# Kernel optimization log

Measured on AMD Instinct MI355X. Metric: run time of the kernel, lower is better.

Reference implementation:

```python
import jax, jax.numpy as jnp
import numpy as np
import math

B, S, E, NH = 1024, 16, 32, 4  # batch, seq, attn embed dim, heads
H = 64                          # lstm1 hidden; lstm2 hidden = H//2 = E


def _pos_encoding(s, d):
    pos = jnp.arange(s, dtype=jnp.float32)[:, None]
    div = jnp.exp(jnp.arange(0, d, 2, dtype=jnp.float32) * (-math.log(10000.0) / d))
    pe = jnp.zeros((s, d), jnp.float32)
    pe = pe.at[:, 0::2].set(jnp.sin(pos * div))
    pe = pe.at[:, 1::2].set(jnp.cos(pos * div))
    return pe


def _lstm(x, wih, whh, bih, bhh):
    # x: [B,S,in]; PyTorch gate order i,f,g,o; h0=c0=0
    b = x.shape[0]
    h_dim = whh.shape[1]
    xg = jnp.einsum('bsi,gi->bsg', x, wih) + bih + bhh  # precompute input contribution

    def step(carry, xt):
        h, c = carry
        g = xt + h @ whh.T
        i, f, gg, o = jnp.split(g, 4, axis=-1)
        c = jax.nn.sigmoid(f) * c + jax.nn.sigmoid(i) * jnp.tanh(gg)
        h = jax.nn.sigmoid(o) * jnp.tanh(c)
        return (h, c), h

    h0 = jnp.zeros((b, h_dim), x.dtype)
    _, hs = jax.lax.scan(step, (h0, h0), jnp.swapaxes(xg, 0, 1))
    return jnp.swapaxes(hs, 0, 1)  # [B,S,H]


def setup_inputs() -> dict:
    key = jax.random.key(0)
    ks = jax.random.split(key, 24)

    def rn(k, shape, s=0.15):
        return jax.random.normal(k, shape, jnp.float32) * s

    return {
        'x': jax.random.normal(ks[0], (B, S, 1), jnp.float32),
        'emb_w': rn(ks[1], (32, 1)), 'emb_b': rn(ks[2], (32,), 0.05),
        'l1_wih': rn(ks[3], (4 * H, 32)), 'l1_whh': rn(ks[4], (4 * H, H)),
        'l1_bih': rn(ks[5], (4 * H,), 0.05), 'l1_bhh': rn(ks[6], (4 * H,), 0.05),
        'l2_wih': rn(ks[7], (4 * (H // 2), H)), 'l2_whh': rn(ks[8], (4 * (H // 2), H // 2)),
        'l2_bih': rn(ks[9], (4 * (H // 2),), 0.05), 'l2_bhh': rn(ks[10], (4 * (H // 2),), 0.05),
        'attn_w': rn(ks[11], (3 * E, E)), 'attn_b': rn(ks[12], (3 * E,), 0.05),
        'attn_ow': rn(ks[13], (E, E)), 'attn_ob': rn(ks[14], (E,), 0.05),
        'd1_w': rn(ks[15], (64, E)), 'd1_b': rn(ks[16], (64,), 0.05),
        'bn1_g': jnp.ones((64,), jnp.float32), 'bn1_b': jnp.zeros((64,), jnp.float32),
        'd2_w': rn(ks[17], (32, 64)), 'd2_b': rn(ks[18], (32,), 0.05),
        'bn2_g': jnp.ones((32,), jnp.float32), 'bn2_b': jnp.zeros((32,), jnp.float32),
        'd3_w': rn(ks[19], (1, 32)), 'd3_b': rn(ks[20], (1,), 0.05),
    }


def reference(x, emb_w, emb_b, l1_wih, l1_whh, l1_bih, l1_bhh,
              l2_wih, l2_whh, l2_bih, l2_bhh,
              attn_w, attn_b, attn_ow, attn_ob,
              d1_w, d1_b, bn1_g, bn1_b, d2_w, d2_b, bn2_g, bn2_b, d3_w, d3_b):
    eps = 1e-5
    h = x @ emb_w.T + emb_b                      # [B,S,32]
    h = h + _pos_encoding(h.shape[1], h.shape[2])
    l1 = _lstm(h, l1_wih, l1_whh, l1_bih, l1_bhh)          # [B,S,64]  (dropout: eval -> id)
    l2 = _lstm(l1, l2_wih, l2_whh, l2_bih, l2_bhh)         # [B,S,32]
    l2 = l2 + l1[:, :, :l2.shape[2]]                        # residual

    # nn.MultiheadAttention with default batch_first=False: attends over axis 0 (=B here),
    # faithful to the original module's behavior.
    L, N, _ = l2.shape
    hd = E // NH
    qkv = l2 @ attn_w.T + attn_b
    q, k, v = jnp.split(qkv, 3, axis=-1)
    q = q.reshape(L, N, NH, hd) * (1.0 / math.sqrt(hd))
    k = k.reshape(L, N, NH, hd)
    v = v.reshape(L, N, NH, hd)
    scores = jnp.einsum('lnhd,mnhd->nhlm', q, k)           # [S,4,B,B]
    a = jax.nn.softmax(scores, axis=-1)
    att = jnp.einsum('nhlm,mnhd->lnhd', a, v).reshape(L, N, E)
    att = att @ attn_ow.T + attn_ob

    z = att[:, -1, :]                                       # [B,32]

    def bn(t, g, b):  # eval-mode BatchNorm1d with fresh running stats (mean=0, var=1)
        return t * (g / jnp.sqrt(1.0 + eps)) + b

    z = jax.nn.relu(bn(z @ d1_w.T + d1_b, bn1_g, bn1_b))
    z = jax.nn.relu(bn(z @ d2_w.T + d2_b, bn2_g, bn2_b))
    return jax.nn.sigmoid(z @ d3_w.T + d3_b)                # [B,1]
```

## Files before the change

### kernel.cpp

```cpp
#include <hip/hip_runtime.h>
#include <math.h>


typedef __attribute__((ext_vector_type(8))) short short8v;
typedef __attribute__((ext_vector_type(4))) float f32x4;

__device__ __forceinline__ float sigf(float x) { return 1.0f / (1.0f + __expf(-x)); }
__device__ __forceinline__ float tanh_f(float x) {
    float a = fabsf(x);
    float e = __expf(2.0f * a);
    float t = 1.0f - 2.0f / (e + 1.0f);
    return copysignf(t, x);
}
__device__ __forceinline__ unsigned short f2bf(float f) {
    unsigned int u = __float_as_uint(f);
    unsigned int r = (u + 0x7FFFu + ((u >> 16) & 1u)) >> 16;
    return (unsigned short)r;
}

__global__ __launch_bounds__(256, 1) void lstm_kernel(
    const float* __restrict__ x,
    const float* __restrict__ emb_w, const float* __restrict__ emb_b,
    const float* __restrict__ wih1, const float* __restrict__ whh1,
    const float* __restrict__ bih1, const float* __restrict__ bhh1,
    const float* __restrict__ wih2, const float* __restrict__ whh2,
    const float* __restrict__ bih2, const float* __restrict__ bhh2,
    const float* __restrict__ attn_w, const float* __restrict__ attn_b,
    float* __restrict__ Q, float* __restrict__ K, float* __restrict__ V) {
    const int tid = threadIdx.x;
    const int w = tid >> 6, lane = tid & 63;
    const int l15 = lane & 15, q4 = lane >> 4;
    const int base = blockIdx.x * 16;

    __shared__ __align__(16) unsigned char E_raw[16 * 1024];
    __shared__ __align__(16) unsigned char H1_raw[2][2048];
    __shared__ __align__(16) unsigned char H2_raw[2][1024];
    __shared__ __align__(16) unsigned char WF2[24 * 1024];
    __shared__ __align__(16) float L1F[16][64];
    __shared__ __align__(16) float L2F[16][32];

    const unsigned jx7 = (unsigned)(l15 & 7) << 4;
    const unsigned jx4 = (unsigned)(l15 & 3) << 4;

    short8v w1f[4][3];
#pragma unroll
    for (int t = 0; t < 4; t++) {
        const int row = (w + 4 * t) * 16 + l15;
#pragma unroll
        for (int sl = 0; sl < 3; sl++) {
            short8v f;
#pragma unroll
            for (int e = 0; e < 8; e++) {
                int k = sl * 32 + q4 * 8 + e;
                float v = (k < 64) ? whh1[row * 64 + k] : wih1[row * 32 + (k - 64)];
                f[e] = (short)f2bf(v);
            }
            w1f[t][sl] = f;
        }
    }

    for (int f = w; f < 24; f += 4) {
        int t2 = f / 3, sl = f - t2 * 3;
        int row = t2 * 16 + l15;
        int koff = sl * 32 + q4 * 8;
        const float* src = (sl < 2) ? (wih2 + row * 64 + koff) : (whh2 + row * 32 + (koff - 64));
        float4 va = *(const float4*)(src);
        float4 vb = *(const float4*)(src + 4);
        short8v pk;
        pk[0] = (short)f2bf(va.x); pk[1] = (short)f2bf(va.y);
        pk[2] = (short)f2bf(va.z); pk[3] = (short)f2bf(va.w);
        pk[4] = (short)f2bf(vb.x); pk[5] = (short)f2bf(vb.y);
        pk[6] = (short)f2bf(vb.z); pk[7] = (short)f2bf(vb.w);
        *(short8v*)(&WF2[f * 1024 + lane * 16]) = pk;
    }

    float b1r[4][4];
#pragma unroll
    for (int t = 0; t < 4; t++)
#pragma unroll
        for (int e = 0; e < 4; e++) {
            int r = (w + 4 * t) * 16 + q4 * 4 + e;
            b1r[t][e] = bih1[r] + bhh1[r];
        }
    float b2r[4][4];
#pragma unroll
    for (int t = 0; t < 4; t++)
#pragma unroll
        for (int e = 0; e < 4; e++) {
            int r = ((w & 1) + 2 * t) * 16 + q4 * 4 + e;
            b2r[t][e] = bih2[r] + bhh2[r];
        }

    *(unsigned long long*)(H1_raw[0] + tid * 8) = 0ULL;
    if (tid < 128) *(unsigned long long*)(H2_raw[0] + tid * 8) = 0ULL;
    {
        const int je = tid >> 4, se = tid & 15;
        float xv = x[(base + je) * 16 + se];
        float ev[32];
#pragma unroll
        for (int ii = 0; ii < 16; ii++) {
            float d = __expf(-0.28782313662425574f * (float)(2 * ii));
            float ang = (float)se * d;
            ev[2 * ii] = xv * emb_w[2 * ii] + emb_b[2 * ii] + __sinf(ang);
            ev[2 * ii + 1] = xv * emb_w[2 * ii + 1] + emb_b[2 * ii + 1] + __cosf(ang);
        }
        unsigned jm = (unsigned)(je & 3) << 4;
#pragma unroll
        for (int b = 0; b < 4; b++) {
            short8v pk;
#pragma unroll
            for (int e = 0; e < 8; e++) pk[e] = (short)f2bf(ev[b * 8 + e]);
            *(short8v*)(&E_raw[se * 1024 + je * 64 + (((unsigned)(b * 16)) ^ jm)]) = pk;
        }
    }
    float c1[4] = {0.f, 0.f, 0.f, 0.f};
    float c2[4] = {0.f, 0.f, 0.f, 0.f};
    __syncthreads();

    const int u0 = w * 16 + q4 * 4;
    const int u20 = w * 16 + q4 * 4;

#define L2FRAG(T, SL) (*(const short8v*)(&WF2[(((w + 2 * (T)) * 3 + (SL)) << 10) + lane * 16]))

#pragma unroll 2
    for (int s = 0; s < 16; s++) {
        const int p = s & 1, pn = p ^ 1;
        const unsigned char* H1p = H1_raw[p];
        unsigned char* H1n = H1_raw[pn];
        short8v B0 = *(const short8v*)(H1p + (((unsigned)(l15 * 128 + q4 * 16)) ^ jx7));
        short8v B1 = *(const short8v*)(H1p + (((unsigned)(l15 * 128 + 64 + q4 * 16)) ^ jx7));
        short8v BE = *(const short8v*)(&E_raw[s * 1024] + (((unsigned)(l15 * 64 + q4 * 16)) ^ jx4));
        f32x4 a0 = {b1r[0][0], b1r[0][1], b1r[0][2], b1r[0][3]};
        f32x4 a1 = {b1r[1][0], b1r[1][1], b1r[1][2], b1r[1][3]};
        f32x4 a2 = {b1r[2][0], b1r[2][1], b1r[2][2], b1r[2][3]};
        f32x4 a3 = {b1r[3][0], b1r[3][1], b1r[3][2], b1r[3][3]};
        a0 = __builtin_amdgcn_mfma_f32_16x16x32_bf16(w1f[0][0], B0, a0, 0, 0, 0);
        a1 = __builtin_amdgcn_mfma_f32_16x16x32_bf16(w1f[1][0], B0, a1, 0, 0, 0);
        a2 = __builtin_amdgcn_mfma_f32_16x16x32_bf16(w1f[2][0], B0, a2, 0, 0, 0);
        a3 = __builtin_amdgcn_mfma_f32_16x16x32_bf16(w1f[3][0], B0, a3, 0, 0, 0);
        a0 = __builtin_amdgcn_mfma_f32_16x16x32_bf16(w1f[0][1], B1, a0, 0, 0, 0);
        a1 = __builtin_amdgcn_mfma_f32_16x16x32_bf16(w1f[1][1], B1, a1, 0, 0, 0);
        a2 = __builtin_amdgcn_mfma_f32_16x16x32_bf16(w1f[2][1], B1, a2, 0, 0, 0);
        a3 = __builtin_amdgcn_mfma_f32_16x16x32_bf16(w1f[3][1], B1, a3, 0, 0, 0);
        a0 = __builtin_amdgcn_mfma_f32_16x16x32_bf16(w1f[0][2], BE, a0, 0, 0, 0);
        a1 = __builtin_amdgcn_mfma_f32_16x16x32_bf16(w1f[1][2], BE, a1, 0, 0, 0);
        a2 = __builtin_amdgcn_mfma_f32_16x16x32_bf16(w1f[2][2], BE, a2, 0, 0, 0);
        a3 = __builtin_amdgcn_mfma_f32_16x16x32_bf16(w1f[3][2], BE, a3, 0, 0, 0);
        float h1v[4];
#pragma unroll
        for (int e = 0; e < 4; e++) {
            c1[e] = sigf(a1[e]) * c1[e] + sigf(a0[e]) * tanh_f(a2[e]);
            h1v[e] = sigf(a3[e]) * tanh_f(c1[e]);
        }
        {
            unsigned long long pk =
                (unsigned long long)f2bf(h1v[0]) | ((unsigned long long)f2bf(h1v[1]) << 16) |
                ((unsigned long long)f2bf(h1v[2]) << 32) | ((unsigned long long)f2bf(h1v[3]) << 48);
            *(unsigned long long*)(H1n + (((unsigned)(l15 * 128 + u0 * 2)) ^ jx7)) = pk;
        }
        if (s == 15) *(float4*)(&L1F[l15][u0]) = make_float4(h1v[0], h1v[1], h1v[2], h1v[3]);
        __syncthreads();
        if (w < 2) {
            const unsigned char* H2p = H2_raw[p];
            short8v C0 = *(const short8v*)(H1n + (((unsigned)(l15 * 128 + q4 * 16)) ^ jx7));
            short8v C1f = *(const short8v*)(H1n + (((unsigned)(l15 * 128 + 64 + q4 * 16)) ^ jx7));
            short8v C2 = *(const short8v*)(H2p + (((unsigned)(l15 * 64 + q4 * 16)) ^ jx4));
            f32x4 d0 = {b2r[0][0], b2r[0][1], b2r[0][2], b2r[0][3]};
            f32x4 d1 = {b2r[1][0], b2r[1][1], b2r[1][2], b2r[1][3]};
            f32x4 d2 = {b2r[2][0], b2r[2][1], b2r[2][2], b2r[2][3]};
            f32x4 d3 = {b2r[3][0], b2r[3][1], b2r[3][2], b2r[3][3]};
            d0 = __builtin_amdgcn_mfma_f32_16x16x32_bf16(L2FRAG(0, 0), C0, d0, 0, 0, 0);
            d1 = __builtin_amdgcn_mfma_f32_16x16x32_bf16(L2FRAG(1, 0), C0, d1, 0, 0, 0);
            d2 = __builtin_amdgcn_mfma_f32_16x16x32_bf16(L2FRAG(2, 0), C0, d2, 0, 0, 0);
            d3 = __builtin_amdgcn_mfma_f32_16x16x32_bf16(L2FRAG(3, 0), C0, d3, 0, 0, 0);
            d0 = __builtin_amdgcn_mfma_f32_16x16x32_bf16(L2FRAG(0, 1), C1f, d0, 0, 0, 0);
            d1 = __builtin_amdgcn_mfma_f32_16x16x32_bf16(L2FRAG(1, 1), C1f, d1, 0, 0, 0);
            d2 = __builtin_amdgcn_mfma_f32_16x16x32_bf16(L2FRAG(2, 1), C1f, d2, 0, 0, 0);
            d3 = __builtin_amdgcn_mfma_f32_16x16x32_bf16(L2FRAG(3, 1), C1f, d3, 0, 0, 0);
            d0 = __builtin_amdgcn_mfma_f32_16x16x32_bf16(L2FRAG(0, 2), C2, d0, 0, 0, 0);
            d1 = __builtin_amdgcn_mfma_f32_16x16x32_bf16(L2FRAG(1, 2), C2, d1, 0, 0, 0);
            d2 = __builtin_amdgcn_mfma_f32_16x16x32_bf16(L2FRAG(2, 2), C2, d2, 0, 0, 0);
            d3 = __builtin_amdgcn_mfma_f32_16x16x32_bf16(L2FRAG(3, 2), C2, d3, 0, 0, 0);
            float h2v[4];
#pragma unroll
            for (int e = 0; e < 4; e++) {
                c2[e] = sigf(d1[e]) * c2[e] + sigf(d0[e]) * tanh_f(d2[e]);
                h2v[e] = sigf(d3[e]) * tanh_f(c2[e]);
            }
            unsigned long long pk =
                (unsigned long long)f2bf(h2v[0]) | ((unsigned long long)f2bf(h2v[1]) << 16) |
                ((unsigned long long)f2bf(h2v[2]) << 32) | ((unsigned long long)f2bf(h2v[3]) << 48);
            *(unsigned long long*)(H2_raw[pn] + (((unsigned)(l15 * 64 + u20 * 2)) ^ jx4)) = pk;
            if (s == 15) *(float4*)(&L2F[l15][u20]) = make_float4(h2v[0], h2v[1], h2v[2], h2v[3]);
        }
        __syncthreads();
    }

    {
        const int j = tid >> 4, rb = tid & 15;
        const int gb = base + j;
        const float4* l1p = (const float4*)(&L1F[j][0]);
        const float4* l2p = (const float4*)(&L2F[j][0]);
#pragma unroll
        for (int rep = 0; rep < 6; rep++) {
            int row = rb + 16 * rep;
            float acc = attn_b[row];
            const float4* wrow = (const float4*)(attn_w + row * 32);
#pragma unroll
            for (int k4 = 0; k4 < 8; k4++) {
                float4 lv1 = l1p[k4];
                float4 lv2 = l2p[k4];
                float4 ww = wrow[k4];
                float lx = lv2.x + lv1.x, ly = lv2.y + lv1.y, lz = lv2.z + lv1.z, lw = lv2.w + lv1.w;
                acc += lx * ww.x + ly * ww.y + lz * ww.z + lw * ww.w;
            }
            if (row < 32) Q[gb * 32 + row] = acc * 0.35355339059327373f;
            else if (row < 64) K[gb * 32 + (row - 32)] = acc;
            else V[gb * 32 + (row - 64)] = acc;
        }
    }
#undef L2FRAG
}

__global__ __launch_bounds__(256, 2) void attn_kernel(
    const float* __restrict__ Q, const float* __restrict__ K, const float* __restrict__ V,
    float* __restrict__ pm, float* __restrict__ ps, float* __restrict__ pacc) {
    int c = blockIdx.x & 15, lt = blockIdx.x >> 4;
    int t = threadIdx.x;
    int h = t >> 6, l = lt * 64 + (t & 63);
    __shared__ __align__(16) float Ks[64 * 32];
    __shared__ __align__(16) float Vs[64 * 32];
    {
        const float4* Kg = (const float4*)(K + c * 2048);
        const float4* Vg = (const float4*)(V + c * 2048);
        float4* K4 = (float4*)Ks;
        float4* V4 = (float4*)Vs;
        K4[t] = Kg[t];
        K4[t + 256] = Kg[t + 256];
        V4[t] = Vg[t];
        V4[t + 256] = Vg[t + 256];
    }
    const float4* qg = (const float4*)(Q + l * 32 + h * 8);
    float4 q0 = qg[0], q1 = qg[1];
    __syncthreads();
    float m_r = -1e30f, l_r = 0.f;
    float4 acc0 = {0, 0, 0, 0}, acc1 = {0, 0, 0, 0};
#pragma unroll 4
    for (int m = 0; m < 64; m++) {
        const float4* k4 = (const float4*)(Ks + m * 32 + h * 8);
        float4 ka = k4[0], kb = k4[1];
        float s = q0.x * ka.x + q0.y * ka.y + q0.z * ka.z + q0.w * ka.w +
                  q1.x * kb.x + q1.y * kb.y + q1.z * kb.z + q1.w * kb.w;
        const float4* v4 = (const float4*)(Vs + m * 32 + h * 8);
        float4 va = v4[0], vb = v4[1];
        float nm = fmaxf(m_r, s);
        float f = __expf(m_r - nm);
        float pp = __expf(s - nm);
        l_r = l_r * f + pp;
        acc0.x = acc0.x * f + pp * va.x;
        acc0.y = acc0.y * f + pp * va.y;
        acc0.z = acc0.z * f + pp * va.z;
        acc0.w = acc0.w * f + pp * va.w;
        acc1.x = acc1.x * f + pp * vb.x;
        acc1.y = acc1.y * f + pp * vb.y;
        acc1.z = acc1.z * f + pp * vb.z;
        acc1.w = acc1.w * f + pp * vb.w;
        m_r = nm;
    }
    int idx = (c * 4 + h) * 1024 + l;
    pm[idx] = m_r;
    ps[idx] = l_r;
    float4* po = (float4*)(pacc + idx * 8);
    po[0] = acc0;
    po[1] = acc1;
}

__global__ __launch_bounds__(256) void head_kernel(
    const float* __restrict__ pm, const float* __restrict__ ps, const float* __restrict__ pacc,
    const float* __restrict__ ow, const float* __restrict__ ob,
    const float* __restrict__ d1w, const float* __restrict__ d1b,
    const float* __restrict__ g1, const float* __restrict__ b1,
    const float* __restrict__ d2w, const float* __restrict__ d2b,
    const float* __restrict__ g2, const float* __restrict__ b2,
    const float* __restrict__ d3w, const float* __restrict__ d3b,
    float* __restrict__ out) {
    int wid = threadIdx.x >> 6, j = threadIdx.x & 63;
    int l = blockIdx.x * 4 + wid;
    __shared__ float att_s[4][32], z_s[4][32], r1s[4][64];
    if (j < 32) {
        int h = j >> 3, d = j & 7;
        float M = -1e30f;
#pragma unroll
        for (int c = 0; c < 16; c++) M = fmaxf(M, pm[(c * 4 + h) * 1024 + l]);
        float den = 0.f, num = 0.f;
#pragma unroll
        for (int c = 0; c < 16; c++) {
            int idx = (c * 4 + h) * 1024 + l;
            float e = __expf(pm[idx] - M);
            den += e * ps[idx];
            num += e * pacc[idx * 8 + d];
        }
        att_s[wid][j] = num / den;
    }
    __syncthreads();
    if (j < 32) {
        float a = ob[j];
#pragma unroll
        for (int i = 0; i < 32; i++) a += att_s[wid][i] * ow[j * 32 + i];
        z_s[wid][j] = a;
    }
    __syncthreads();
    const float inv = rsqrtf(1.0f + 1e-5f);
    if (j < 64) {
        float a = d1b[j];
#pragma unroll
        for (int i = 0; i < 32; i++) a += z_s[wid][i] * d1w[j * 32 + i];
        a = a * (g1[j] * inv) + b1[j];
        r1s[wid][j] = fmaxf(a, 0.f);
    }
    __syncthreads();
    if (j < 32) {
        float a = d2b[j];
#pragma unroll
        for (int i = 0; i < 64; i++) a += r1s[wid][i] * d2w[j * 64 + i];
        a = a * (g2[j] * inv) + b2[j];
        float r2 = fmaxf(a, 0.f);
        float p = r2 * d3w[j];
        p += __shfl_down(p, 16);
        p += __shfl_down(p, 8);
        p += __shfl_down(p, 4);
        p += __shfl_down(p, 2);
        p += __shfl_down(p, 1);
        if (j == 0) out[l] = 1.0f / (1.0f + __expf(-(p + d3b[0])));
    }
}

extern "C" void kernel_launch(void* const* d_in, const int* in_sizes, int n_in,
                              void* d_out, int out_size, void* d_ws, size_t ws_size,
                              hipStream_t stream) {
    const float* x      = (const float*)d_in[0];
    const float* emb_w  = (const float*)d_in[1];
    const float* emb_b  = (const float*)d_in[2];
    const float* l1_wih = (const float*)d_in[3];
    const float* l1_whh = (const float*)d_in[4];
    const float* l1_bih = (const float*)d_in[5];
    const float* l1_bhh = (const float*)d_in[6];
    const float* l2_wih = (const float*)d_in[7];
    const float* l2_whh = (const float*)d_in[8];
    const float* l2_bih = (const float*)d_in[9];
    const float* l2_bhh = (const float*)d_in[10];
    const float* attn_w = (const float*)d_in[11];
    const float* attn_b = (const float*)d_in[12];
    const float* attn_ow = (const float*)d_in[13];
    const float* attn_ob = (const float*)d_in[14];
    const float* d1_w  = (const float*)d_in[15];
    const float* d1_b  = (const float*)d_in[16];
    const float* bn1_g = (const float*)d_in[17];
    const float* bn1_b = (const float*)d_in[18];
    const float* d2_w  = (const float*)d_in[19];
    const float* d2_b  = (const float*)d_in[20];
    const float* bn2_g = (const float*)d_in[21];
    const float* bn2_b = (const float*)d_in[22];
    const float* d3_w  = (const float*)d_in[23];
    const float* d3_b  = (const float*)d_in[24];
    float* out = (float*)d_out;

    float* ws   = (float*)d_ws;
    float* Q    = ws;
    float* K    = ws + 32768;
    float* V    = ws + 65536;
    float* pm   = ws + 98304;
    float* ps   = ws + 163840;
    float* pacc = ws + 229376;

    lstm_kernel<<<64, 256, 0, stream>>>(x, emb_w, emb_b, l1_wih, l1_whh, l1_bih, l1_bhh,
                                        l2_wih, l2_whh, l2_bih, l2_bhh,
                                        attn_w, attn_b, Q, K, V);
    attn_kernel<<<256, 256, 0, stream>>>(Q, K, V, pm, ps, pacc);
    head_kernel<<<256, 256, 0, stream>>>(pm, ps, pacc, attn_ow, attn_ob, d1_w, d1_b,
                                         bn1_g, bn1_b, d2_w, d2_b, bn2_g, bn2_b,
                                         d3_w, d3_b, out);
}
```

Before: 162.5 us.

## Skew LSTM layers to one barrier per step and fuse attention with head

The LSTM loop is restructured so that layer 2 at step s runs alongside layer 1 at step s+1. Both read the same H1 buffer, which removes one of the two barriers per timestep and lets layer 2 reuse layer 1's loaded fragments. The attention and head kernels are merged into one kernel in which each wave scans all keys directly from global memory and reduces the partial softmax states with shuffles, removing the partial-result buffers and one launch. Sigmoid and tanh now use the hardware reciprocal, and bf16 packing uses v_cvt_pk_bf16_f32; both change rounding slightly, and the fused attention now reads K and V from global/L2 in every block.

```diff
diff --git a/kernel.cpp b/kernel.cpp
--- a/kernel.cpp
+++ b/kernel.cpp
@@ -5,17 +5,25 @@
 typedef __attribute__((ext_vector_type(8))) short short8v;
 typedef __attribute__((ext_vector_type(4))) float f32x4;
 
-__device__ __forceinline__ float sigf(float x) { return 1.0f / (1.0f + __expf(-x)); }
+__device__ __forceinline__ float sigf(float x) {
+    float e = __expf(-x);
+    return __builtin_amdgcn_rcpf(1.0f + e);
+}
 __device__ __forceinline__ float tanh_f(float x) {
     float a = fabsf(x);
     float e = __expf(2.0f * a);
-    float t = 1.0f - 2.0f / (e + 1.0f);
+    float t = 1.0f - 2.0f * __builtin_amdgcn_rcpf(e + 1.0f);
     return copysignf(t, x);
 }
 __device__ __forceinline__ unsigned short f2bf(float f) {
     unsigned int u = __float_as_uint(f);
     unsigned int r = (u + 0x7FFFu + ((u >> 16) & 1u)) >> 16;
     return (unsigned short)r;
+}
+__device__ __forceinline__ unsigned cvtpk_bf16(float lo, float hi) {
+    unsigned r;
+    asm("v_cvt_pk_bf16_f32 %0, %1, %2" : "=v"(r) : "v"(lo), "v"(hi));
+    return r;
 }
 
 __global__ __launch_bounds__(256, 1) void lstm_kernel(
@@ -91,8 +99,8 @@
             b2r[t][e] = bih2[r] + bhh2[r];
         }
 
-    *(unsigned long long*)(H1_raw[0] + tid * 8) = 0ULL;
-    if (tid < 128) *(unsigned long long*)(H2_raw[0] + tid * 8) = 0ULL;
+    *(unsigned long long*)(H1_raw[1] + tid * 8) = 0ULL;
+    if (tid < 128) *(unsigned long long*)(H2_raw[1] + tid * 8) = 0ULL;
     {
         const int je = tid >> 4, se = tid & 15;
         float xv = x[(base + je) * 16 + se];
@@ -115,25 +123,24 @@
     }
     float c1[4] = {0.f, 0.f, 0.f, 0.f};
     float c2[4] = {0.f, 0.f, 0.f, 0.f};
-    __syncthreads();
 
     const int u0 = w * 16 + q4 * 4;
-    const int u20 = w * 16 + q4 * 4;
-
+
+#define LDBE(S)  (*(const short8v*)(&E_raw[(S) * 1024] + (((unsigned)(l15 * 64 + q4 * 16)) ^ jx4)))
+#define LDB0(HP) (*(const short8v*)((HP) + (((unsigned)(l15 * 128 + q4 * 16)) ^ jx7)))
+#define LDB1(HP) (*(const short8v*)((HP) + (((unsigned)(l15 * 128 + 64 + q4 * 16)) ^ jx7)))
+#define LDC2(HP) (*(const short8v*)((HP) + (((unsigned)(l15 * 64 + q4 * 16)) ^ jx4)))
 #define L2FRAG(T, SL) (*(const short8v*)(&WF2[(((w + 2 * (T)) * 3 + (SL)) << 10) + lane * 16]))
 
-#pragma unroll 2
-    for (int s = 0; s < 16; s++) {
-        const int p = s & 1, pn = p ^ 1;
-        const unsigned char* H1p = H1_raw[p];
-        unsigned char* H1n = H1_raw[pn];
-        short8v B0 = *(const short8v*)(H1p + (((unsigned)(l15 * 128 + q4 * 16)) ^ jx7));
-        short8v B1 = *(const short8v*)(H1p + (((unsigned)(l15 * 128 + 64 + q4 * 16)) ^ jx7));
-        short8v BE = *(const short8v*)(&E_raw[s * 1024] + (((unsigned)(l15 * 64 + q4 * 16)) ^ jx4));
+    auto phase1 = [&](unsigned char* H1n, short8v BE, short8v B0, short8v B1, bool last) {
         f32x4 a0 = {b1r[0][0], b1r[0][1], b1r[0][2], b1r[0][3]};
         f32x4 a1 = {b1r[1][0], b1r[1][1], b1r[1][2], b1r[1][3]};
         f32x4 a2 = {b1r[2][0], b1r[2][1], b1r[2][2], b1r[2][3]};
         f32x4 a3 = {b1r[3][0], b1r[3][1], b1r[3][2], b1r[3][3]};
+        a0 = __builtin_amdgcn_mfma_f32_16x16x32_bf16(w1f[0][2], BE, a0, 0, 0, 0);
+        a1 = __builtin_amdgcn_mfma_f32_16x16x32_bf16(w1f[1][2], BE, a1, 0, 0, 0);
+        a2 = __builtin_amdgcn_mfma_f32_16x16x32_bf16(w1f[2][2], BE, a2, 0, 0, 0);
+        a3 = __builtin_amdgcn_mfma_f32_16x16x32_bf16(w1f[3][2], BE, a3, 0, 0, 0);
         a0 = __builtin_amdgcn_mfma_f32_16x16x32_bf16(w1f[0][0], B0, a0, 0, 0, 0);
         a1 = __builtin_amdgcn_mfma_f32_16x16x32_bf16(w1f[1][0], B0, a1, 0, 0, 0);
         a2 = __builtin_amdgcn_mfma_f32_16x16x32_bf16(w1f[2][0], B0, a2, 0, 0, 0);
@@ -142,41 +149,41 @@
         a1 = __builtin_amdgcn_mfma_f32_16x16x32_bf16(w1f[1][1], B1, a1, 0, 0, 0);
         a2 = __builtin_amdgcn_mfma_f32_16x16x32_bf16(w1f[2][1], B1, a2, 0, 0, 0);
         a3 = __builtin_amdgcn_mfma_f32_16x16x32_bf16(w1f[3][1], B1, a3, 0, 0, 0);
-        a0 = __builtin_amdgcn_mfma_f32_16x16x32_bf16(w1f[0][2], BE, a0, 0, 0, 0);
-        a1 = __builtin_amdgcn_mfma_f32_16x16x32_bf16(w1f[1][2], BE, a1, 0, 0, 0);
-        a2 = __builtin_amdgcn_mfma_f32_16x16x32_bf16(w1f[2][2], BE, a2, 0, 0, 0);
-        a3 = __builtin_amdgcn_mfma_f32_16x16x32_bf16(w1f[3][2], BE, a3, 0, 0, 0);
         float h1v[4];
 #pragma unroll
         for (int e = 0; e < 4; e++) {
             c1[e] = sigf(a1[e]) * c1[e] + sigf(a0[e]) * tanh_f(a2[e]);
             h1v[e] = sigf(a3[e]) * tanh_f(c1[e]);
         }
-        {
-            unsigned long long pk =
-                (unsigned long long)f2bf(h1v[0]) | ((unsigned long long)f2bf(h1v[1]) << 16) |
-                ((unsigned long long)f2bf(h1v[2]) << 32) | ((unsigned long long)f2bf(h1v[3]) << 48);
-            *(unsigned long long*)(H1n + (((unsigned)(l15 * 128 + u0 * 2)) ^ jx7)) = pk;
-        }
-        if (s == 15) *(float4*)(&L1F[l15][u0]) = make_float4(h1v[0], h1v[1], h1v[2], h1v[3]);
+        uint2 pk = make_uint2(cvtpk_bf16(h1v[0], h1v[1]), cvtpk_bf16(h1v[2], h1v[3]));
+        *(uint2*)(H1n + (((unsigned)(l15 * 128 + u0 * 2)) ^ jx7)) = pk;
+        if (last) *(float4*)(&L1F[l15][u0]) = make_float4(h1v[0], h1v[1], h1v[2], h1v[3]);
+    };
+
+    __syncthreads();
+    phase1(H1_raw[0], LDBE(0), LDB0(H1_raw[1]), LDB1(H1_raw[1]), false);
+
+#pragma unroll 2
+    for (int s = 0; s < 16; s++) {
+        const int p = s & 1;
         __syncthreads();
+        short8v BEn = LDBE((s < 15) ? (s + 1) : 15);
+        short8v B0 = LDB0(H1_raw[p]);
+        short8v B1 = LDB1(H1_raw[p]);
         if (w < 2) {
-            const unsigned char* H2p = H2_raw[p];
-            short8v C0 = *(const short8v*)(H1n + (((unsigned)(l15 * 128 + q4 * 16)) ^ jx7));
-            short8v C1f = *(const short8v*)(H1n + (((unsigned)(l15 * 128 + 64 + q4 * 16)) ^ jx7));
-            short8v C2 = *(const short8v*)(H2p + (((unsigned)(l15 * 64 + q4 * 16)) ^ jx4));
+            short8v C2 = LDC2(H2_raw[p ^ 1]);
             f32x4 d0 = {b2r[0][0], b2r[0][1], b2r[0][2], b2r[0][3]};
             f32x4 d1 = {b2r[1][0], b2r[1][1], b2r[1][2], b2r[1][3]};
             f32x4 d2 = {b2r[2][0], b2r[2][1], b2r[2][2], b2r[2][3]};
             f32x4 d3 = {b2r[3][0], b2r[3][1], b2r[3][2], b2r[3][3]};
-            d0 = __builtin_amdgcn_mfma_f32_16x16x32_bf16(L2FRAG(0, 0), C0, d0, 0, 0, 0);
-            d1 = __builtin_amdgcn_mfma_f32_16x16x32_bf16(L2FRAG(1, 0), C0, d1, 0, 0, 0);
-            d2 = __builtin_amdgcn_mfma_f32_16x16x32_bf16(L2FRAG(2, 0), C0, d2, 0, 0, 0);
-            d3 = __builtin_amdgcn_mfma_f32_16x16x32_bf16(L2FRAG(3, 0), C0, d3, 0, 0, 0);
-            d0 = __builtin_amdgcn_mfma_f32_16x16x32_bf16(L2FRAG(0, 1), C1f, d0, 0, 0, 0);
-            d1 = __builtin_amdgcn_mfma_f32_16x16x32_bf16(L2FRAG(1, 1), C1f, d1, 0, 0, 0);
-            d2 = __builtin_amdgcn_mfma_f32_16x16x32_bf16(L2FRAG(2, 1), C1f, d2, 0, 0, 0);
-            d3 = __builtin_amdgcn_mfma_f32_16x16x32_bf16(L2FRAG(3, 1), C1f, d3, 0, 0, 0);
+            d0 = __builtin_amdgcn_mfma_f32_16x16x32_bf16(L2FRAG(0, 0), B0, d0, 0, 0, 0);
+            d1 = __builtin_amdgcn_mfma_f32_16x16x32_bf16(L2FRAG(1, 0), B0, d1, 0, 0, 0);
+            d2 = __builtin_amdgcn_mfma_f32_16x16x32_bf16(L2FRAG(2, 0), B0, d2, 0, 0, 0);
+            d3 = __builtin_amdgcn_mfma_f32_16x16x32_bf16(L2FRAG(3, 0), B0, d3, 0, 0, 0);
+            d0 = __builtin_amdgcn_mfma_f32_16x16x32_bf16(L2FRAG(0, 1), B1, d0, 0, 0, 0);
+            d1 = __builtin_amdgcn_mfma_f32_16x16x32_bf16(L2FRAG(1, 1), B1, d1, 0, 0, 0);
+            d2 = __builtin_amdgcn_mfma_f32_16x16x32_bf16(L2FRAG(2, 1), B1, d2, 0, 0, 0);
+            d3 = __builtin_amdgcn_mfma_f32_16x16x32_bf16(L2FRAG(3, 1), B1, d3, 0, 0, 0);
             d0 = __builtin_amdgcn_mfma_f32_16x16x32_bf16(L2FRAG(0, 2), C2, d0, 0, 0, 0);
             d1 = __builtin_amdgcn_mfma_f32_16x16x32_bf16(L2FRAG(1, 2), C2, d1, 0, 0, 0);
             d2 = __builtin_amdgcn_mfma_f32_16x16x32_bf16(L2FRAG(2, 2), C2, d2, 0, 0, 0);
@@ -187,15 +194,14 @@
                 c2[e] = sigf(d1[e]) * c2[e] + sigf(d0[e]) * tanh_f(d2[e]);
                 h2v[e] = sigf(d3[e]) * tanh_f(c2[e]);
             }
-            unsigned long long pk =
-                (unsigned long long)f2bf(h2v[0]) | ((unsigned long long)f2bf(h2v[1]) << 16) |
-                ((unsigned long long)f2bf(h2v[2]) << 32) | ((unsigned long long)f2bf(h2v[3]) << 48);
-            *(unsigned long long*)(H2_raw[pn] + (((unsigned)(l15 * 64 + u20 * 2)) ^ jx4)) = pk;
-            if (s == 15) *(float4*)(&L2F[l15][u20]) = make_float4(h2v[0], h2v[1], h2v[2], h2v[3]);
-        }
-        __syncthreads();
-    }
-
+            uint2 pk = make_uint2(cvtpk_bf16(h2v[0], h2v[1]), cvtpk_bf16(h2v[2], h2v[3]));
+            *(uint2*)(H2_raw[p] + (((unsigned)(l15 * 64 + u0 * 2)) ^ jx4)) = pk;
+            if (s == 15) *(float4*)(&L2F[l15][u0]) = make_float4(h2v[0], h2v[1], h2v[2], h2v[3]);
+        }
+        if (s < 15) phase1(H1_raw[p ^ 1], BEn, B0, B1, (s + 1) == 15);
+    }
+
+    __syncthreads();
     {
         const int j = tid >> 4, rb = tid & 15;
         const int gb = base + j;
@@ -219,44 +225,43 @@
             else V[gb * 32 + (row - 64)] = acc;
         }
     }
+#undef LDBE
+#undef LDB0
+#undef LDB1
+#undef LDC2
 #undef L2FRAG
 }
 
-__global__ __launch_bounds__(256, 2) void attn_kernel(
+__global__ __launch_bounds__(256) void attn_head_kernel(
     const float* __restrict__ Q, const float* __restrict__ K, const float* __restrict__ V,
-    float* __restrict__ pm, float* __restrict__ ps, float* __restrict__ pacc) {
-    int c = blockIdx.x & 15, lt = blockIdx.x >> 4;
-    int t = threadIdx.x;
-    int h = t >> 6, l = lt * 64 + (t & 63);
-    __shared__ __align__(16) float Ks[64 * 32];
-    __shared__ __align__(16) float Vs[64 * 32];
-    {
-        const float4* Kg = (const float4*)(K + c * 2048);
-        const float4* Vg = (const float4*)(V + c * 2048);
-        float4* K4 = (float4*)Ks;
-        float4* V4 = (float4*)Vs;
-        K4[t] = Kg[t];
-        K4[t + 256] = Kg[t + 256];
-        V4[t] = Vg[t];
-        V4[t + 256] = Vg[t + 256];
-    }
-    const float4* qg = (const float4*)(Q + l * 32 + h * 8);
-    float4 q0 = qg[0], q1 = qg[1];
-    __syncthreads();
-    float m_r = -1e30f, l_r = 0.f;
+    const float* __restrict__ ow, const float* __restrict__ ob,
+    const float* __restrict__ d1w, const float* __restrict__ d1b,
+    const float* __restrict__ g1, const float* __restrict__ bn1b,
+    const float* __restrict__ d2w, const float* __restrict__ d2b,
+    const float* __restrict__ g2, const float* __restrict__ bn2b,
+    const float* __restrict__ d3w, const float* __restrict__ d3b,
+    float* __restrict__ out) {
+    int wid = threadIdx.x >> 6, lane = threadIdx.x & 63;
+    int l = blockIdx.x * 4 + wid;
+    int h = lane >> 4, ks = lane & 15;
+    __shared__ float att_s[4][32], z_s[4][32], r1s[4][64];
+
+    const float4* qp = (const float4*)(Q + l * 32 + h * 8);
+    float4 q0 = qp[0], q1 = qp[1];
+    float m = -1e30f, den = 0.f;
     float4 acc0 = {0, 0, 0, 0}, acc1 = {0, 0, 0, 0};
 #pragma unroll 4
-    for (int m = 0; m < 64; m++) {
-        const float4* k4 = (const float4*)(Ks + m * 32 + h * 8);
-        float4 ka = k4[0], kb = k4[1];
+    for (int t = 0; t < 64; t++) {
+        int key = t * 16 + ks;
+        const float4* kp = (const float4*)(K + key * 32 + h * 8);
+        float4 ka = kp[0], kb = kp[1];
+        const float4* vp = (const float4*)(V + key * 32 + h * 8);
+        float4 va = vp[0], vb = vp[1];
         float s = q0.x * ka.x + q0.y * ka.y + q0.z * ka.z + q0.w * ka.w +
                   q1.x * kb.x + q1.y * kb.y + q1.z * kb.z + q1.w * kb.w;
-        const float4* v4 = (const float4*)(Vs + m * 32 + h * 8);
-        float4 va = v4[0], vb = v4[1];
-        float nm = fmaxf(m_r, s);
-        float f = __expf(m_r - nm);
-        float pp = __expf(s - nm);
-        l_r = l_r * f + pp;
+        float nm = fmaxf(m, s);
+        float f = __expf(m - nm), pp = __expf(s - nm);
+        den = den * f + pp;
         acc0.x = acc0.x * f + pp * va.x;
         acc0.y = acc0.y * f + pp * va.y;
         acc0.z = acc0.z * f + pp * va.z;
@@ -265,65 +270,74 @@
         acc1.y = acc1.y * f + pp * vb.y;
         acc1.z = acc1.z * f + pp * vb.z;
         acc1.w = acc1.w * f + pp * vb.w;
-        m_r = nm;
-    }
-    int idx = (c * 4 + h) * 1024 + l;
-    pm[idx] = m_r;
-    ps[idx] = l_r;
-    float4* po = (float4*)(pacc + idx * 8);
-    po[0] = acc0;
-    po[1] = acc1;
-}
-
-__global__ __launch_bounds__(256) void head_kernel(
-    const float* __restrict__ pm, const float* __restrict__ ps, const float* __restrict__ pacc,
-    const float* __restrict__ ow, const float* __restrict__ ob,
-    const float* __restrict__ d1w, const float* __restrict__ d1b,
-    const float* __restrict__ g1, const float* __restrict__ b1,
-    const float* __restrict__ d2w, const float* __restrict__ d2b,
-    const float* __restrict__ g2, const float* __restrict__ b2,
-    const float* __restrict__ d3w, const float* __restrict__ d3b,
-    float* __restrict__ out) {
-    int wid = threadIdx.x >> 6, j = threadIdx.x & 63;
-    int l = blockIdx.x * 4 + wid;
-    __shared__ float att_s[4][32], z_s[4][32], r1s[4][64];
-    if (j < 32) {
-        int h = j >> 3, d = j & 7;
-        float M = -1e30f;
-#pragma unroll
-        for (int c = 0; c < 16; c++) M = fmaxf(M, pm[(c * 4 + h) * 1024 + l]);
-        float den = 0.f, num = 0.f;
-#pragma unroll
-        for (int c = 0; c < 16; c++) {
-            int idx = (c * 4 + h) * 1024 + l;
-            float e = __expf(pm[idx] - M);
-            den += e * ps[idx];
-            num += e * pacc[idx * 8 + d];
-        }
-        att_s[wid][j] = num / den;
-    }
-    __syncthreads();
+        m = nm;
+    }
+#pragma unroll
+    for (int d = 1; d < 16; d <<= 1) {
+        float m2 = __shfl_xor(m, d), den2 = __shfl_xor(den, d);
+        float4 b0, b1;
+        b0.x = __shfl_xor(acc0.x, d); b0.y = __shfl_xor(acc0.y, d);
+        b0.z = __shfl_xor(acc0.z, d); b0.w = __shfl_xor(acc0.w, d);
+        b1.x = __shfl_xor(acc1.x, d); b1.y = __shfl_xor(acc1.y, d);
+        b1.z = __shfl_xor(acc1.z, d); b1.w = __shfl_xor(acc1.w, d);
+        float nm = fmaxf(m, m2);
+        float f = __expf(m - nm), f2 = __expf(m2 - nm);
+        den = den * f + den2 * f2;
+        acc0.x = acc0.x * f + b0.x * f2;
+        acc0.y = acc0.y * f + b0.y * f2;
+        acc0.z = acc0.z * f + b0.z * f2;
+        acc0.w = acc0.w * f + b0.w * f2;
+        acc1.x = acc1.x * f + b1.x * f2;
+        acc1.y = acc1.y * f + b1.y * f2;
+        acc1.z = acc1.z * f + b1.z * f2;
+        acc1.w = acc1.w * f + b1.w * f2;
+        m = nm;
+    }
+    float r = __builtin_amdgcn_rcpf(den);
+    if (ks == 0) {
+        float4 o0 = make_float4(acc0.x * r, acc0.y * r, acc0.z * r, acc0.w * r);
+        float4 o1 = make_float4(acc1.x * r, acc1.y * r, acc1.z * r, acc1.w * r);
+        *(float4*)(&att_s[wid][h * 8]) = o0;
+        *(float4*)(&att_s[wid][h * 8 + 4]) = o1;
+    }
+    __syncthreads();
+    int j = lane;
     if (j < 32) {
         float a = ob[j];
-#pragma unroll
-        for (int i = 0; i < 32; i++) a += att_s[wid][i] * ow[j * 32 + i];
+        const float4* aw = (const float4*)(&att_s[wid][0]);
+        const float4* wr = (const float4*)(ow + j * 32);
+#pragma unroll
+        for (int k4 = 0; k4 < 8; k4++) {
+            float4 u = aw[k4], wv = wr[k4];
+            a += u.x * wv.x + u.y * wv.y + u.z * wv.z + u.w * wv.w;
+        }
         z_s[wid][j] = a;
     }
     __syncthreads();
     const float inv = rsqrtf(1.0f + 1e-5f);
-    if (j < 64) {
+    {
         float a = d1b[j];
-#pragma unroll
-        for (int i = 0; i < 32; i++) a += z_s[wid][i] * d1w[j * 32 + i];
-        a = a * (g1[j] * inv) + b1[j];
+        const float4* zw = (const float4*)(&z_s[wid][0]);
+        const float4* wr = (const float4*)(d1w + j * 32);
+#pragma unroll
+        for (int k4 = 0; k4 < 8; k4++) {
+            float4 u = zw[k4], wv = wr[k4];
+            a += u.x * wv.x + u.y * wv.y + u.z * wv.z + u.w * wv.w;
+        }
+        a = a * (g1[j] * inv) + bn1b[j];
         r1s[wid][j] = fmaxf(a, 0.f);
     }
     __syncthreads();
     if (j < 32) {
         float a = d2b[j];
-#pragma unroll
-        for (int i = 0; i < 64; i++) a += r1s[wid][i] * d2w[j * 64 + i];
-        a = a * (g2[j] * inv) + b2[j];
+        const float4* rw = (const float4*)(&r1s[wid][0]);
+        const float4* wr = (const float4*)(d2w + j * 64);
+#pragma unroll
+        for (int k4 = 0; k4 < 16; k4++) {
+            float4 u = rw[k4], wv = wr[k4];
+            a += u.x * wv.x + u.y * wv.y + u.z * wv.z + u.w * wv.w;
+        }
+        a = a * (g2[j] * inv) + bn2b[j];
         float r2 = fmaxf(a, 0.f);
         float p = r2 * d3w[j];
         p += __shfl_down(p, 16);
@@ -331,7 +345,7 @@
         p += __shfl_down(p, 4);
         p += __shfl_down(p, 2);
         p += __shfl_down(p, 1);
-        if (j == 0) out[l] = 1.0f / (1.0f + __expf(-(p + d3b[0])));
+        if (j == 0) out[l] = __builtin_amdgcn_rcpf(1.0f + __expf(-(p + d3b[0])));
     }
 }
 
@@ -365,19 +379,15 @@
     const float* d3_b  = (const float*)d_in[24];
     float* out = (float*)d_out;
 
-    float* ws   = (float*)d_ws;
-    float* Q    = ws;
-    float* K    = ws + 32768;
-    float* V    = ws + 65536;
-    float* pm   = ws + 98304;
-    float* ps   = ws + 163840;
-    float* pacc = ws + 229376;
+    float* ws = (float*)d_ws;
+    float* Q  = ws;
+    float* K  = ws + 32768;
+    float* V  = ws + 65536;
 
     lstm_kernel<<<64, 256, 0, stream>>>(x, emb_w, emb_b, l1_wih, l1_whh, l1_bih, l1_bhh,
                                         l2_wih, l2_whh, l2_bih, l2_bhh,
                                         attn_w, attn_b, Q, K, V);
-    attn_kernel<<<256, 256, 0, stream>>>(Q, K, V, pm, ps, pacc);
-    head_kernel<<<256, 256, 0, stream>>>(pm, ps, pacc, attn_ow, attn_ob, d1_w, d1_b,
-                                         bn1_g, bn1_b, d2_w, d2_b, bn2_g, bn2_b,
-                                         d3_w, d3_b, out);
-}
+    attn_head_kernel<<<256, 256, 0, stream>>>(Q, K, V, attn_ow, attn_ob, d1_w, d1_b,
+                                              bn1_g, bn1_b, d2_w, d2_b, bn2_g, bn2_b,
+                                              d3_w, d3_b, out);
+}
```

Measured after the change: 175.9 us. +8.3%, slower.
